# Optimization experiments

Measured on AMD Instinct MI355X. Metric: run time of the kernel, lower is better.

The kernel has to match this reference:

```python
import jax, jax.numpy as jnp
import numpy as np

# Scatter2Operator config (matches init_kwargs)
NUM_HEADS = 16   # dims[2] / glob_size
GLOB_SIZE = 64
HEAD_SIZE = 64   # dims[2] / num_heads


def setup_inputs() -> dict:
    key = jax.random.key(0)
    ks = jax.random.split(key, 6)
    B, N, G, D0, D2 = 8, 4096, 64, 1024, 1024
    scale = 0.02
    return {
        "x0": jax.random.normal(ks[0], (B, G, D0), jnp.float32),
        "x2": jax.random.normal(ks[1], (B, N, D2), jnp.float32),
        "Wk": jax.random.normal(ks[2], (NUM_HEADS * GLOB_SIZE, D2), jnp.float32) * scale,
        "Wp": jax.random.normal(ks[3], (NUM_HEADS * HEAD_SIZE, D0), jnp.float32) * scale,
        "Wo": jax.random.normal(ks[4], (D2, NUM_HEADS * HEAD_SIZE), jnp.float32) * scale,
        "bo": jnp.zeros((D2,), jnp.float32),
    }


def reference(x0, x2, Wk, Wp, Wo, bo):
    # x2: [B, N, D2] -> kernel scores; x0: [B, G, D0] -> premise values.
    B, N, _ = x2.shape
    H, G, Dh = NUM_HEADS, GLOB_SIZE, HEAD_SIZE
    # kernel = softmax over glob slots (dropout is identity in eval mode)
    k = jnp.einsum('bnd,kd->bnk', x2, Wk).reshape(B, N, H, G)
    k = jax.nn.softmax(k, axis=-1)                      # [B, N, H, G]
    # premise projection: [B, G, H, Dh]
    p = jnp.einsum('bgd,kd->bgk', x0, Wp).reshape(B, G, H, Dh)
    # attention-like gather over the G global slots, per head
    pred = jnp.einsum('bnhg,bghd->bnhd', k, p)          # [B, N, H, Dh]
    pred = pred.reshape(B, N, H * Dh)
    # writer linear (with bias)
    return jnp.einsum('bnk,dk->bnd', pred, Wo) + bo
```

## Files before the change

### kernel.cpp

```cpp
#include <hip/hip_runtime.h>


using bf16x8 = __attribute__((ext_vector_type(8))) __bf16;
using f32x4  = __attribute__((ext_vector_type(4))) float;

__device__ __forceinline__ unsigned short f2b(float f) {
  unsigned u = __float_as_uint(f);
  u += 0x7fffu + ((u >> 16) & 1u);
  return (unsigned short)(u >> 16);
}

__global__ void cvt_all(const float* __restrict__ x2, unsigned short* __restrict__ x2b, int n0,
                        const float* __restrict__ x0, unsigned short* __restrict__ x0b, int n1,
                        const float* __restrict__ Wk, unsigned short* __restrict__ Wkb, int n2,
                        const float* __restrict__ Wp, unsigned short* __restrict__ Wpb, int n3,
                        const float* __restrict__ Wo, unsigned short* __restrict__ Wob, int n4)
{
  const int ntot = n0 + n1 + n2 + n3 + n4;
  int i = blockIdx.x * blockDim.x + threadIdx.x;
  const int stride = gridDim.x * blockDim.x;
  for (; i < ntot; i += stride) {
    const float* src; unsigned short* dst; int j = i;
    if (j < n0) { src = x2; dst = x2b; }
    else if ((j -= n0) < n1) { src = x0; dst = x0b; }
    else if ((j -= n1) < n2) { src = Wk; dst = Wkb; }
    else if ((j -= n2) < n3) { src = Wp; dst = Wpb; }
    else { j -= n3; src = Wo; dst = Wob; }
    float4 v = reinterpret_cast<const float4*>(src)[j];
    ushort4 o;
    o.x = f2b(v.x); o.y = f2b(v.y); o.z = f2b(v.z); o.w = f2b(v.w);
    reinterpret_cast<ushort4*>(dst)[j] = o;
  }
}

#define GLOAD_LDS(gsrc, ldst) __builtin_amdgcn_global_load_lds(                 \
    (const __attribute__((address_space(1))) unsigned int*)(gsrc),              \
    (__attribute__((address_space(3))) unsigned int*)(ldst), 16, 0, 0)

__device__ __forceinline__ void glds16(const unsigned short* g, unsigned ldsoff) {
  asm volatile("s_mov_b32 m0, %0\n\t"
               "global_load_lds_dwordx4 %1, off"
               :: "s"(ldsoff), "v"(g) : "memory");
}

#define BM 128
#define BN 128
#define BK 32

template<int EPI>
__launch_bounds__(256)
__global__ void gemm_bt(const unsigned short* __restrict__ A,
                        const unsigned short* __restrict__ B,
                        void* __restrict__ Cv,
                        const float* __restrict__ bias,
                        int M, int N, int K, int lda, int ldb, int ldc,
                        int batch2,
                        long sA1, long sA2, long sB1, long sB2, long sC1, long sC2)
{
  __shared__ __align__(16) unsigned short As[BM * BK];
  __shared__ __align__(16) unsigned short Bs[BN * BK];

  const int z  = blockIdx.z;
  const int z1 = z / batch2, z2 = z - z1 * batch2;
  const unsigned short* Ab = A + z1 * sA1 + z2 * sA2;
  const unsigned short* Bb = B + z1 * sB1 + z2 * sB2;
  const long cbase = z1 * sC1 + z2 * sC2;

  const int tid  = threadIdx.x;
  const int lane = tid & 63;
  const int wid  = tid >> 6;
  const int wr   = (wid >> 1) * 64;
  const int wc   = (wid & 1) * 64;
  const int brow = blockIdx.x * BM;
  const int bcol = blockIdx.y * BN;
  const int lr   = lane & 15;
  const int ko   = (lane >> 4) * 8;

  f32x4 acc[4][4] = {};

  const int t1  = tid + 256;
  const int r0  = tid >> 2, kc0 = (tid & 3) * 8;
  const int r1  = t1 >> 2,  kc1 = (t1 & 3) * 8;
  int ar0 = brow + r0; if (ar0 >= M) ar0 = M - 1;
  int ar1 = brow + r1; if (ar1 >= M) ar1 = M - 1;
  int br0 = bcol + r0; if (br0 >= N) br0 = N - 1;
  int br1 = bcol + r1; if (br1 >= N) br1 = N - 1;
  const unsigned short* a0p = Ab + (long)ar0 * lda + kc0;
  const unsigned short* a1p = Ab + (long)ar1 * lda + kc1;
  const unsigned short* b0p = Bb + (long)br0 * ldb + kc0;
  const unsigned short* b1p = Bb + (long)br1 * ldb + kc1;

  for (int kt = 0; kt < K; kt += BK) {
    __syncthreads();
    GLOAD_LDS(a0p + kt, &As[tid * 8]);
    GLOAD_LDS(a1p + kt, &As[t1 * 8]);
    GLOAD_LDS(b0p + kt, &Bs[tid * 8]);
    GLOAD_LDS(b1p + kt, &Bs[t1 * 8]);
    __syncthreads();

    bf16x8 af[4], bfr[4];
#pragma unroll
    for (int m = 0; m < 4; ++m)
      af[m] = *reinterpret_cast<const bf16x8*>(&As[(wr + m * 16 + lr) * BK + ko]);
#pragma unroll
    for (int n = 0; n < 4; ++n)
      bfr[n] = *reinterpret_cast<const bf16x8*>(&Bs[(wc + n * 16 + lr) * BK + ko]);
#pragma unroll
    for (int m = 0; m < 4; ++m)
#pragma unroll
      for (int n = 0; n < 4; ++n)
        acc[m][n] = __builtin_amdgcn_mfma_f32_16x16x32_bf16(af[m], bfr[n], acc[m][n], 0, 0, 0);
  }

  const int rowb = brow + wr + (lane >> 4) * 4;
  const int colb = bcol + wc + lr;

  if (EPI == 1) {
    float* C = (float*)Cv + cbase;
#pragma unroll
    for (int n = 0; n < 4; ++n) {
      int col = colb + n * 16;
      if (col >= N) continue;
      float bv = bias ? bias[col] : 0.0f;
#pragma unroll
      for (int m = 0; m < 4; ++m)
#pragma unroll
        for (int r = 0; r < 4; ++r) {
          int row = rowb + m * 16 + r;
          if (row < M) C[(long)row * ldc + col] = acc[m][n][r] + bv;
        }
    }
  } else {
    unsigned short* C = (unsigned short*)Cv + cbase;
#pragma unroll
    for (int n = 0; n < 4; ++n) {
      int col = colb + n * 16;
      if (col >= N) continue;
#pragma unroll
      for (int m = 0; m < 4; ++m)
#pragma unroll
        for (int r = 0; r < 4; ++r) {
          int row = rowb + m * 16 + r;
          if (row < M) C[(long)row * ldc + col] = f2b(acc[m][n][r]);
        }
    }
  }
}


#define BARRIER() __builtin_amdgcn_s_barrier()
#define VMC4()   asm volatile("s_waitcnt vmcnt(4)" ::: "memory")
#define VMC0()   asm volatile("s_waitcnt vmcnt(0)" ::: "memory")


__launch_bounds__(512)
__global__ void gemm256_g1p(const unsigned short* __restrict__ A0,
                            const unsigned short* __restrict__ B0,
                            unsigned short* __restrict__ C0,
                            const unsigned short* __restrict__ A1,
                            const unsigned short* __restrict__ B1,
                            unsigned short* __restrict__ C1,
                            int K)
{
  extern __shared__ __align__(16) char smem[];

  const int tid  = threadIdx.x;
  const int lane = tid & 63, wid = tid >> 6;
  const int wm = wid >> 2, wn = wid & 3;
  const int lr = lane & 15, hi = lane >> 4;
  const int swz  = (lane & 7) << 4;
  const int prow = lane >> 3;
  const int pxor = ((lane & 7) ^ prow) * 8;

  const int bid = blockIdx.x;
  int bx, by, epi;
  const unsigned short* Ab; const unsigned short* Bb; unsigned short* Cb;
  if (bid < 512) {
    const int lin = (bid & 7) * 64 + (bid >> 3);
    bx = lin >> 2; by = lin & 3;
    epi = 2; Ab = A0; Bb = B0; Cb = C0;
  } else {
    const int r = bid - 512;
    bx = r >> 2; by = r & 3;
    epi = 0; Ab = A1; Bb = B1; Cb = C1;
  }
  const int brow = bx * 256, bcol = by * 256;

  unsigned short* ldsA[2] = { (unsigned short*)(smem),
                              (unsigned short*)(smem + 65536) };
  unsigned short* ldsB[2] = { (unsigned short*)(smem + 32768),
                              (unsigned short*)(smem + 98304) };
  const unsigned ldsbase =
      __builtin_amdgcn_readfirstlane((unsigned)(unsigned long long)smem);

  const long ldaL = 1024, ldbL = 1024, ldcL = 1024;

  auto stageA = [&](int buf, int h, int kt) {
    const unsigned short* s = Ab + (long)(brow + h * 128 + wid * 8 + prow) * ldaL + kt + pxor;
    unsigned d = ldsbase + (unsigned)(buf * 65536 + h * 16384 + wid * 1024);
    glds16(s, __builtin_amdgcn_readfirstlane(d));
    glds16(s + 64 * ldaL, __builtin_amdgcn_readfirstlane(d + 8192u));
  };
  auto stageB = [&](int buf, int h, int kt) {
    const unsigned short* s = Bb + (long)(bcol + h * 128 + wid * 8 + prow) * ldbL + kt + pxor;
    unsigned d = ldsbase + (unsigned)(32768 + buf * 65536 + h * 16384 + wid * 1024);
    glds16(s, __builtin_amdgcn_readfirstlane(d));
    glds16(s + 64 * ldbL, __builtin_amdgcn_readfirstlane(d + 8192u));
  };

  bf16x8 afr[4][2], bfr[4][2];
  auto ldA_ = [&](int buf, int mh) {
    const unsigned short* base = ldsA[buf];
#pragma unroll
    for (int mi = 0; mi < 4; ++mi) {
      const int row = wm * 128 + mh * 64 + mi * 16 + lr;
#pragma unroll
      for (int ks = 0; ks < 2; ++ks) {
        const int cb = (ks * 64 + hi * 16) ^ swz;
        afr[mi][ks] = *(const bf16x8*)(base + row * 64 + (cb >> 1));
      }
    }
  };
  auto ldB_ = [&](int buf, int nh) {
    const unsigned short* base = ldsB[buf];
#pragma unroll
    for (int ni = 0; ni < 2; ++ni) {
      const int row = wn * 64 + nh * 32 + ni * 16 + lr;
#pragma unroll
      for (int ks = 0; ks < 2; ++ks) {
        const int cb = (ks * 64 + hi * 16) ^ swz;
        bfr[nh * 2 + ni][ks] = *(const bf16x8*)(base + row * 64 + (cb >> 1));
      }
    }
  };

  f32x4 acc[8][4] = {};
  auto mmaQ = [&](int mh, int nh) {
    __builtin_amdgcn_s_setprio(1);
#pragma unroll
    for (int ks = 0; ks < 2; ++ks)
#pragma unroll
      for (int mi = 0; mi < 4; ++mi)
#pragma unroll
        for (int ni = 0; ni < 2; ++ni)
          acc[mh * 4 + mi][nh * 2 + ni] = __builtin_amdgcn_mfma_f32_16x16x32_bf16(
              afr[mi][ks], bfr[nh * 2 + ni][ks], acc[mh * 4 + mi][nh * 2 + ni], 0, 0, 0);
    __builtin_amdgcn_s_setprio(0);
  };

  stageB(0, 0, 0); stageB(0, 1, 0); stageA(0, 0, 0); stageA(0, 1, 0);
  stageB(1, 0, 64); stageB(1, 1, 64);
  VMC4(); BARRIER();

  const int NI = K >> 7;
#pragma unroll 1
  for (int i = 0; i < NI; ++i) {
    const int kt1 = i * 128 + 64;
    int kt2 = i * 128 + 128; if (kt2 >= K) kt2 -= K;
    int kt3 = i * 128 + 192; if (kt3 >= K) kt3 -= K;

    ldA_(0, 0); ldB_(0, 0); ldB_(0, 1); stageA(1, 0, kt1);
    BARRIER(); mmaQ(0, 0); BARRIER();
    stageA(1, 1, kt1);
    BARRIER(); mmaQ(0, 1); BARRIER();
    ldA_(0, 1); stageB(0, 0, kt2);
    BARRIER(); mmaQ(1, 0); BARRIER();
    stageB(0, 1, kt2); VMC4();
    BARRIER(); mmaQ(1, 1); BARRIER();
    ldA_(1, 0); ldB_(1, 0); ldB_(1, 1); stageA(0, 0, kt2);
    BARRIER(); mmaQ(0, 0); BARRIER();
    stageA(0, 1, kt2);
    BARRIER(); mmaQ(0, 1); BARRIER();
    ldA_(1, 1); stageB(1, 0, kt3);
    BARRIER(); mmaQ(1, 0); BARRIER();
    stageB(1, 1, kt3); VMC4();
    BARRIER(); mmaQ(1, 1); BARRIER();
  }
  VMC0();

  const int rowb = brow + wm * 128 + hi * 4;
  const int colb = bcol + wn * 64 + lr;

  if (epi == 2) {
#pragma unroll
    for (int m = 0; m < 8; ++m) {
#pragma unroll
      for (int r = 0; r < 4; ++r) {
        float v0 = acc[m][0][r], v1 = acc[m][1][r], v2 = acc[m][2][r], v3 = acc[m][3][r];
        float mx = fmaxf(fmaxf(v0, v1), fmaxf(v2, v3));
        mx = fmaxf(mx, __shfl_xor(mx, 1));
        mx = fmaxf(mx, __shfl_xor(mx, 2));
        mx = fmaxf(mx, __shfl_xor(mx, 4));
        mx = fmaxf(mx, __shfl_xor(mx, 8));
        float e0 = __expf(v0 - mx), e1 = __expf(v1 - mx);
        float e2 = __expf(v2 - mx), e3 = __expf(v3 - mx);
        float s = e0 + e1 + e2 + e3;
        s += __shfl_xor(s, 1);
        s += __shfl_xor(s, 2);
        s += __shfl_xor(s, 4);
        s += __shfl_xor(s, 8);
        float inv = 1.0f / s;
        unsigned short* cp = Cb + (long)(rowb + m * 16 + r) * ldcL + colb;
        cp[0]  = f2b(e0 * inv);
        cp[16] = f2b(e1 * inv);
        cp[32] = f2b(e2 * inv);
        cp[48] = f2b(e3 * inv);
      }
    }
  } else {
#pragma unroll
    for (int n = 0; n < 4; ++n) {
      const int col = colb + n * 16;
#pragma unroll
      for (int m = 0; m < 8; ++m)
#pragma unroll
        for (int r = 0; r < 4; ++r)
          Cb[(long)(rowb + m * 16 + r) * ldcL + col] = f2b(acc[m][n][r]);
    }
  }
}

__launch_bounds__(512)
__global__ void gemm256_out(const unsigned short* __restrict__ A,
                            const unsigned short* __restrict__ B,
                            float* __restrict__ C,
                            const float* __restrict__ bias,
                            int K, long sA, long sB, long sC)
{
  extern __shared__ __align__(16) char smem[];

  const int tid  = threadIdx.x;
  const int lane = tid & 63, wid = tid >> 6;
  const int wm = wid >> 2, wn = wid & 3;
  const int lr = lane & 15, hi = lane >> 4;
  const int swz  = (lane & 7) << 4;
  const int prow = lane >> 3;
  const int pxor = ((lane & 7) ^ prow) * 8;

  const int bid = blockIdx.x;
  const int z = bid & 7, idx = bid >> 3;
  const int bx = idx & 15, by = idx >> 4;
  const int brow = bx * 256, bcol = by * 256;
  const unsigned short* __restrict__ Ab = A + (long)z * sA;
  const unsigned short* __restrict__ Bb = B + (long)z * sB;
  const long cbase = (long)z * sC;

  unsigned short* ldsA[2] = { (unsigned short*)(smem),
                              (unsigned short*)(smem + 65536) };
  unsigned short* ldsB[2] = { (unsigned short*)(smem + 32768),
                              (unsigned short*)(smem + 98304) };
  const unsigned ldsbase =
      __builtin_amdgcn_readfirstlane((unsigned)(unsigned long long)smem);

  const long ldaL = 1024, ldbL = 1024, ldcL = 1024;

  auto stageA = [&](int buf, int h, int kt) {
    const unsigned short* s = Ab + (long)(brow + h * 128 + wid * 8 + prow) * ldaL + kt + pxor;
    unsigned d = ldsbase + (unsigned)(buf * 65536 + h * 16384 + wid * 1024);
    glds16(s, __builtin_amdgcn_readfirstlane(d));
    glds16(s + 64 * ldaL, __builtin_amdgcn_readfirstlane(d + 8192u));
  };
  auto stageB = [&](int buf, int h, int kt) {
    const unsigned short* s = Bb + (long)(bcol + h * 128 + wid * 8 + prow) * ldbL + kt + pxor;
    unsigned d = ldsbase + (unsigned)(32768 + buf * 65536 + h * 16384 + wid * 1024);
    glds16(s, __builtin_amdgcn_readfirstlane(d));
    glds16(s + 64 * ldbL, __builtin_amdgcn_readfirstlane(d + 8192u));
  };

  bf16x8 afr[4][2], bfr[4][2];
  auto ldA_ = [&](int buf, int mh) {
    const unsigned short* base = ldsA[buf];
#pragma unroll
    for (int mi = 0; mi < 4; ++mi) {
      const int row = wm * 128 + mh * 64 + mi * 16 + lr;
#pragma unroll
      for (int ks = 0; ks < 2; ++ks) {
        const int cb = (ks * 64 + hi * 16) ^ swz;
        afr[mi][ks] = *(const bf16x8*)(base + row * 64 + (cb >> 1));
      }
    }
  };
  auto ldB_ = [&](int buf, int nh) {
    const unsigned short* base = ldsB[buf];
#pragma unroll
    for (int ni = 0; ni < 2; ++ni) {
      const int row = wn * 64 + nh * 32 + ni * 16 + lr;
#pragma unroll
      for (int ks = 0; ks < 2; ++ks) {
        const int cb = (ks * 64 + hi * 16) ^ swz;
        bfr[nh * 2 + ni][ks] = *(const bf16x8*)(base + row * 64 + (cb >> 1));
      }
    }
  };

  f32x4 acc[8][4] = {};
  auto mmaQ = [&](int mh, int nh) {
    __builtin_amdgcn_s_setprio(1);
#pragma unroll
    for (int ks = 0; ks < 2; ++ks)
#pragma unroll
      for (int mi = 0; mi < 4; ++mi)
#pragma unroll
        for (int ni = 0; ni < 2; ++ni)
          acc[mh * 4 + mi][nh * 2 + ni] = __builtin_amdgcn_mfma_f32_16x16x32_bf16(
              afr[mi][ks], bfr[nh * 2 + ni][ks], acc[mh * 4 + mi][nh * 2 + ni], 0, 0, 0);
    __builtin_amdgcn_s_setprio(0);
  };

  stageB(0, 0, 0); stageB(0, 1, 0); stageA(0, 0, 0); stageA(0, 1, 0);
  stageB(1, 0, 64); stageB(1, 1, 64);
  VMC4(); BARRIER();

  const int NI = K >> 7;
#pragma unroll 1
  for (int i = 0; i < NI; ++i) {
    const int kt1 = i * 128 + 64;
    int kt2 = i * 128 + 128; if (kt2 >= K) kt2 -= K;
    int kt3 = i * 128 + 192; if (kt3 >= K) kt3 -= K;

    ldA_(0, 0); ldB_(0, 0); ldB_(0, 1); stageA(1, 0, kt1);
    BARRIER(); mmaQ(0, 0); BARRIER();
    stageA(1, 1, kt1);
    BARRIER(); mmaQ(0, 1); BARRIER();
    ldA_(0, 1); stageB(0, 0, kt2);
    BARRIER(); mmaQ(1, 0); BARRIER();
    stageB(0, 1, kt2); VMC4();
    BARRIER(); mmaQ(1, 1); BARRIER();
    ldA_(1, 0); ldB_(1, 0); ldB_(1, 1); stageA(0, 0, kt2);
    BARRIER(); mmaQ(0, 0); BARRIER();
    stageA(0, 1, kt2);
    BARRIER(); mmaQ(0, 1); BARRIER();
    ldA_(1, 1); stageB(1, 0, kt3);
    BARRIER(); mmaQ(1, 0); BARRIER();
    stageB(1, 1, kt3); VMC4();
    BARRIER(); mmaQ(1, 1); BARRIER();
  }
  VMC0();

  const int rowb = brow + wm * 128 + hi * 4;
  const int colb = bcol + wn * 64 + lr;
  float* Co = C + cbase;
#pragma unroll
  for (int n = 0; n < 4; ++n) {
    const int col = colb + n * 16;
    const float bv = bias[col];
#pragma unroll
    for (int m = 0; m < 8; ++m)
#pragma unroll
      for (int r = 0; r < 4; ++r)
        Co[(long)(rowb + m * 16 + r) * ldcL + col] = acc[m][n][r] + bv;
  }
}

extern "C" void kernel_launch(void* const* d_in, const int* in_sizes, int n_in,
                              void* d_out, int out_size, void* d_ws, size_t ws_size,
                              hipStream_t stream) {
  (void)in_sizes; (void)n_in; (void)out_size; (void)ws_size;
  const float* x0 = (const float*)d_in[0];
  const float* x2 = (const float*)d_in[1];
  const float* Wk = (const float*)d_in[2];
  const float* Wp = (const float*)d_in[3];
  const float* Wo = (const float*)d_in[4];
  const float* bo = (const float*)d_in[5];
  float* out = (float*)d_out;

  const long Bz = 8, Nn = 4096, Gg = 64, Dd = 1024;
  const long MN = Bz * Nn;

  char* ws = (char*)d_ws;
  size_t off = 0;
  auto alloc = [&](size_t bytes) {
    size_t cur = off;
    off = (cur + bytes + 255) & ~(size_t)255;
    return (unsigned short*)(ws + cur);
  };
  unsigned short* x2b = alloc(MN * Dd * 2);
  unsigned short* kb  = alloc(MN * Dd * 2);
  unsigned short* Wkb = alloc(Dd * Dd * 2);
  unsigned short* Wpb = alloc(Dd * Dd * 2);
  unsigned short* Wob = alloc(Dd * Dd * 2);
  unsigned short* x0b = alloc(Bz * Gg * Dd * 2);
  unsigned short* Pb  = alloc(Bz * Gg * Dd * 2);
  unsigned short* Qtb = alloc(Bz * Dd * Dd * 2);

  hipFuncSetAttribute(reinterpret_cast<const void*>(gemm256_g1p),
                      hipFuncAttributeMaxDynamicSharedMemorySize, 131072);
  hipFuncSetAttribute(reinterpret_cast<const void*>(gemm256_out),
                      hipFuncAttributeMaxDynamicSharedMemorySize, 131072);

  cvt_all<<<dim3(4096), dim3(256), 0, stream>>>(
      x2, x2b, (int)(MN * Dd / 4),
      x0, x0b, (int)(Bz * Gg * Dd / 4),
      Wk, Wkb, (int)(Dd * Dd / 4),
      Wp, Wpb, (int)(Dd * Dd / 4),
      Wo, Wob, (int)(Dd * Dd / 4));

  gemm256_g1p<<<dim3(520, 1, 1), dim3(512), 131072, stream>>>(
      x2b, Wkb, kb, x0b, Wpb, Pb, 1024);

  gemm_bt<0><<<dim3(8, 1, 128), dim3(256), 0, stream>>>(
      Wob, Pb, Qtb, nullptr, 1024, 64, 64, 1024, 1024, 1024,
      16, 0, 64, 65536, 64, 1048576, 64);

  gemm256_out<<<dim3(512, 1, 1), dim3(512), 131072, stream>>>(
      kb, Qtb, out, bo, 1024,
      (long)4096 * 1024, (long)1024 * 1024, (long)4096 * 1024);
}
```

Baseline: 239.0 us.

## Double-buffer register fragments and restructure GEMM main loop prefetch schedule

Splits the A and B register fragments into separate ping-pong sets so the next quarter's LDS reads are issued before the current MFMA block rather than immediately after it. Global-to-LDS staging is regrouped in pairs per phase with adjusted vmcnt waits, and the prologue preloads the first fragments. Launch bounds now request two waves per SIMD. The aim is to hide LDS read latency behind MFMAs, at the cost of more VGPRs under a tighter register cap, which may cause spills. The buffer reuse pattern across barriers must stay race-free.

```diff
diff --git a/kernel.cpp b/kernel.cpp
--- a/kernel.cpp
+++ b/kernel.cpp
@@ -147,13 +147,11 @@
   }
 }
 
-
 #define BARRIER() __builtin_amdgcn_s_barrier()
 #define VMC4()   asm volatile("s_waitcnt vmcnt(4)" ::: "memory")
 #define VMC0()   asm volatile("s_waitcnt vmcnt(0)" ::: "memory")
 
-
-__launch_bounds__(512)
+__launch_bounds__(512, 2)
 __global__ void gemm256_g1p(const unsigned short* __restrict__ A0,
                             const unsigned short* __restrict__ B0,
                             unsigned short* __restrict__ C0,
@@ -208,8 +206,10 @@
     glds16(s + 64 * ldbL, __builtin_amdgcn_readfirstlane(d + 8192u));
   };
 
-  bf16x8 afr[4][2], bfr[4][2];
-  auto ldA_ = [&](int buf, int mh) {
+  bf16x8 afr0[4][2], afr1[4][2];
+  bf16x8 bloA[2][2], bloB[2][2], bhi[2][2];
+
+  auto ldA = [&](int buf, int mh, bf16x8 (&dst)[4][2]) {
     const unsigned short* base = ldsA[buf];
 #pragma unroll
     for (int mi = 0; mi < 4; ++mi) {
@@ -217,11 +217,11 @@
 #pragma unroll
       for (int ks = 0; ks < 2; ++ks) {
         const int cb = (ks * 64 + hi * 16) ^ swz;
-        afr[mi][ks] = *(const bf16x8*)(base + row * 64 + (cb >> 1));
+        dst[mi][ks] = *(const bf16x8*)(base + row * 64 + (cb >> 1));
       }
     }
   };
-  auto ldB_ = [&](int buf, int nh) {
+  auto ldB = [&](int buf, int nh, bf16x8 (&dst)[2][2]) {
     const unsigned short* base = ldsB[buf];
 #pragma unroll
     for (int ni = 0; ni < 2; ++ni) {
@@ -229,13 +229,13 @@
 #pragma unroll
       for (int ks = 0; ks < 2; ++ks) {
         const int cb = (ks * 64 + hi * 16) ^ swz;
-        bfr[nh * 2 + ni][ks] = *(const bf16x8*)(base + row * 64 + (cb >> 1));
+        dst[ni][ks] = *(const bf16x8*)(base + row * 64 + (cb >> 1));
       }
     }
   };
 
   f32x4 acc[8][4] = {};
-  auto mmaQ = [&](int mh, int nh) {
+  auto mma = [&](bf16x8 (&a)[4][2], bf16x8 (&b)[2][2], int mh, int nh) {
     __builtin_amdgcn_s_setprio(1);
 #pragma unroll
     for (int ks = 0; ks < 2; ++ks)
@@ -244,13 +244,14 @@
 #pragma unroll
         for (int ni = 0; ni < 2; ++ni)
           acc[mh * 4 + mi][nh * 2 + ni] = __builtin_amdgcn_mfma_f32_16x16x32_bf16(
-              afr[mi][ks], bfr[nh * 2 + ni][ks], acc[mh * 4 + mi][nh * 2 + ni], 0, 0, 0);
+              a[mi][ks], b[ni][ks], acc[mh * 4 + mi][nh * 2 + ni], 0, 0, 0);
     __builtin_amdgcn_s_setprio(0);
   };
 
-  stageB(0, 0, 0); stageB(0, 1, 0); stageA(0, 0, 0); stageA(0, 1, 0);
+  stageA(0, 0, 0); stageA(0, 1, 0); stageB(0, 0, 0); stageB(0, 1, 0);
   stageB(1, 0, 64); stageB(1, 1, 64);
-  VMC4(); BARRIER();
+  VMC0(); BARRIER();
+  ldA(0, 0, afr0); ldB(0, 0, bloA);
 
   const int NI = K >> 7;
 #pragma unroll 1
@@ -259,22 +260,26 @@
     int kt2 = i * 128 + 128; if (kt2 >= K) kt2 -= K;
     int kt3 = i * 128 + 192; if (kt3 >= K) kt3 -= K;
 
-    ldA_(0, 0); ldB_(0, 0); ldB_(0, 1); stageA(1, 0, kt1);
-    BARRIER(); mmaQ(0, 0); BARRIER();
-    stageA(1, 1, kt1);
-    BARRIER(); mmaQ(0, 1); BARRIER();
-    ldA_(0, 1); stageB(0, 0, kt2);
-    BARRIER(); mmaQ(1, 0); BARRIER();
-    stageB(0, 1, kt2); VMC4();
-    BARRIER(); mmaQ(1, 1); BARRIER();
-    ldA_(1, 0); ldB_(1, 0); ldB_(1, 1); stageA(0, 0, kt2);
-    BARRIER(); mmaQ(0, 0); BARRIER();
-    stageA(0, 1, kt2);
-    BARRIER(); mmaQ(0, 1); BARRIER();
-    ldA_(1, 1); stageB(1, 0, kt3);
-    BARRIER(); mmaQ(1, 0); BARRIER();
-    stageB(1, 1, kt3); VMC4();
-    BARRIER(); mmaQ(1, 1); BARRIER();
+    ldB(0, 1, bhi);
+    stageA(1, 0, kt1); stageA(1, 1, kt1); VMC4();
+    BARRIER(); mma(afr0, bloA, 0, 0); BARRIER();
+    ldA(0, 1, afr1);
+    BARRIER(); mma(afr0, bhi, 0, 1); BARRIER();
+    ldB(1, 0, bloB);
+    stageB(0, 0, kt2); stageB(0, 1, kt2); VMC4();
+    BARRIER(); mma(afr1, bloA, 1, 0); BARRIER();
+    ldA(1, 0, afr0);
+    BARRIER(); mma(afr1, bhi, 1, 1); BARRIER();
+    ldB(1, 1, bhi);
+    stageA(0, 0, kt2); stageA(0, 1, kt2); VMC4();
+    BARRIER(); mma(afr0, bloB, 0, 0); BARRIER();
+    ldA(1, 1, afr1);
+    BARRIER(); mma(afr0, bhi, 0, 1); BARRIER();
+    ldB(0, 0, bloA);
+    stageB(1, 0, kt3); stageB(1, 1, kt3); VMC4();
+    BARRIER(); mma(afr1, bloB, 1, 0); BARRIER();
+    ldA(0, 0, afr0);
+    BARRIER(); mma(afr1, bhi, 1, 1); BARRIER();
   }
   VMC0();
 
```

Result: slower. 254.3 us (+6.4%).

## Fuse premise projection into Qt kernel, drop extra blocks from score GEMM

Applied to the files above, without the earlier changes.

The premise projection P = x0·Wp^T, which was computed by 8 extra blocks appended to the score GEMM, moves into a new qtp kernel. qtp computes each per-(batch, head) 64x64 P tile in LDS and immediately multiplies it with a 256-row slice of Wo to produce Qt. This removes the P round-trip through global memory and the generic 128x128 batched GEMM with its padded/clamped tiles, and lets the score GEMM run a uniform 512-block grid. In exchange, each of the 4 bx blocks per (b, h) recomputes the same P tile, which is redundant work.

```diff
diff --git a/kernel.cpp b/kernel.cpp
--- a/kernel.cpp
+++ b/kernel.cpp
@@ -43,124 +43,144 @@
                :: "s"(ldsoff), "v"(g) : "memory");
 }
 
-#define BM 128
-#define BN 128
-#define BK 32
-
-template<int EPI>
+#define BARRIER() __builtin_amdgcn_s_barrier()
+#define VMC4()   asm volatile("s_waitcnt vmcnt(4)" ::: "memory")
+#define VMC0()   asm volatile("s_waitcnt vmcnt(0)" ::: "memory")
+
 __launch_bounds__(256)
-__global__ void gemm_bt(const unsigned short* __restrict__ A,
-                        const unsigned short* __restrict__ B,
-                        void* __restrict__ Cv,
-                        const float* __restrict__ bias,
-                        int M, int N, int K, int lda, int ldb, int ldc,
-                        int batch2,
-                        long sA1, long sA2, long sB1, long sB2, long sC1, long sC2)
+__global__ void qtp(const unsigned short* __restrict__ x0b,
+                    const unsigned short* __restrict__ Wpb,
+                    const unsigned short* __restrict__ Wob,
+                    unsigned short* __restrict__ Qtb)
 {
-  __shared__ __align__(16) unsigned short As[BM * BK];
-  __shared__ __align__(16) unsigned short Bs[BN * BK];
-
+  __shared__ __align__(16) unsigned short Pl[64 * 72];
+  __shared__ __align__(16) unsigned short work[16384];
+
+  const int bx = blockIdx.x;
   const int z  = blockIdx.z;
-  const int z1 = z / batch2, z2 = z - z1 * batch2;
-  const unsigned short* Ab = A + z1 * sA1 + z2 * sA2;
-  const unsigned short* Bb = B + z1 * sB1 + z2 * sB2;
-  const long cbase = z1 * sC1 + z2 * sC2;
+  const int b  = z >> 4, h = z & 15;
 
   const int tid  = threadIdx.x;
   const int lane = tid & 63;
   const int wid  = tid >> 6;
-  const int wr   = (wid >> 1) * 64;
-  const int wc   = (wid & 1) * 64;
-  const int brow = blockIdx.x * BM;
-  const int bcol = blockIdx.y * BN;
   const int lr   = lane & 15;
-  const int ko   = (lane >> 4) * 8;
-
-  f32x4 acc[4][4] = {};
-
-  const int t1  = tid + 256;
-  const int r0  = tid >> 2, kc0 = (tid & 3) * 8;
-  const int r1  = t1 >> 2,  kc1 = (t1 & 3) * 8;
-  int ar0 = brow + r0; if (ar0 >= M) ar0 = M - 1;
-  int ar1 = brow + r1; if (ar1 >= M) ar1 = M - 1;
-  int br0 = bcol + r0; if (br0 >= N) br0 = N - 1;
-  int br1 = bcol + r1; if (br1 >= N) br1 = N - 1;
-  const unsigned short* a0p = Ab + (long)ar0 * lda + kc0;
-  const unsigned short* a1p = Ab + (long)ar1 * lda + kc1;
-  const unsigned short* b0p = Bb + (long)br0 * ldb + kc0;
-  const unsigned short* b1p = Bb + (long)br1 * ldb + kc1;
-
-  for (int kt = 0; kt < K; kt += BK) {
+  const int hi   = lane >> 4;
+
+  const int wr1 = (wid >> 1) * 32, wc1 = (wid & 1) * 32;
+  f32x4 acc1[2][2] = {};
+
+  int srow[2], skc[2];
+#pragma unroll
+  for (int j = 0; j < 2; ++j) {
+    int i = j * 256 + tid;
+    srow[j] = i >> 3;
+    skc[j]  = ((i & 7) ^ (srow[j] & 7)) * 8;
+  }
+  const unsigned short* aSrc = x0b + (long)b * 65536;
+  const unsigned short* bSrc = Wpb + (long)h * 64 * 1024;
+
+  for (int kt = 0; kt < 1024; kt += 64) {
     __syncthreads();
-    GLOAD_LDS(a0p + kt, &As[tid * 8]);
-    GLOAD_LDS(a1p + kt, &As[t1 * 8]);
-    GLOAD_LDS(b0p + kt, &Bs[tid * 8]);
-    GLOAD_LDS(b1p + kt, &Bs[t1 * 8]);
+#pragma unroll
+    for (int j = 0; j < 2; ++j) {
+      int i = j * 256 + tid;
+      GLOAD_LDS(aSrc + (long)srow[j] * 1024 + kt + skc[j], &work[i * 8]);
+      GLOAD_LDS(bSrc + (long)srow[j] * 1024 + kt + skc[j], &work[4096 + i * 8]);
+    }
     __syncthreads();
 
-    bf16x8 af[4], bfr[4];
+    bf16x8 af[2][2], bf[2][2];
+#pragma unroll
+    for (int m = 0; m < 2; ++m) {
+      const int rowA = wr1 + m * 16 + lr;
+      const int rowB = wc1 + m * 16 + lr;
+#pragma unroll
+      for (int ks = 0; ks < 2; ++ks) {
+        const int slotA = ((ks * 4 + hi) ^ (rowA & 7)) * 8;
+        const int slotB = ((ks * 4 + hi) ^ (rowB & 7)) * 8;
+        af[m][ks] = *(const bf16x8*)&work[rowA * 64 + slotA];
+        bf[m][ks] = *(const bf16x8*)&work[4096 + rowB * 64 + slotB];
+      }
+    }
+#pragma unroll
+    for (int ks = 0; ks < 2; ++ks)
+#pragma unroll
+      for (int m = 0; m < 2; ++m)
+#pragma unroll
+        for (int n = 0; n < 2; ++n)
+          acc1[m][n] = __builtin_amdgcn_mfma_f32_16x16x32_bf16(
+              af[m][ks], bf[n][ks], acc1[m][n], 0, 0, 0);
+  }
+
+#pragma unroll
+  for (int m = 0; m < 2; ++m)
+#pragma unroll
+    for (int r = 0; r < 4; ++r) {
+      const int row = wr1 + m * 16 + hi * 4 + r;
+#pragma unroll
+      for (int n = 0; n < 2; ++n)
+        Pl[row * 72 + wc1 + n * 16 + lr] = f2b(acc1[m][n][r]);
+    }
+  __syncthreads();
+
+  const unsigned short* wSrc = Wob + (long)bx * 256 * 1024 + h * 64;
+#pragma unroll
+  for (int j = 0; j < 8; ++j) {
+    int i = j * 256 + tid;
+    int row = i >> 3;
+    int kc  = ((i & 7) ^ (row & 7)) * 8;
+    GLOAD_LDS(wSrc + (long)row * 1024 + kc, &work[i * 8]);
+  }
+  __syncthreads();
+
+  const int wr2 = wid * 64;
+  f32x4 acc2[4][4] = {};
+  bf16x8 af2[4][2], bf2[4][2];
+#pragma unroll
+  for (int m = 0; m < 4; ++m) {
+    const int rowA = wr2 + m * 16 + lr;
+#pragma unroll
+    for (int ks = 0; ks < 2; ++ks) {
+      const int slotA = ((ks * 4 + hi) ^ (rowA & 7)) * 8;
+      af2[m][ks] = *(const bf16x8*)&work[rowA * 64 + slotA];
+    }
+  }
+#pragma unroll
+  for (int n = 0; n < 4; ++n) {
+    const int rowB = n * 16 + lr;
+#pragma unroll
+    for (int ks = 0; ks < 2; ++ks)
+      bf2[n][ks] = *(const bf16x8*)&Pl[rowB * 72 + ks * 32 + hi * 8];
+  }
+#pragma unroll
+  for (int ks = 0; ks < 2; ++ks)
 #pragma unroll
     for (int m = 0; m < 4; ++m)
-      af[m] = *reinterpret_cast<const bf16x8*>(&As[(wr + m * 16 + lr) * BK + ko]);
-#pragma unroll
-    for (int n = 0; n < 4; ++n)
-      bfr[n] = *reinterpret_cast<const bf16x8*>(&Bs[(wc + n * 16 + lr) * BK + ko]);
+#pragma unroll
+      for (int n = 0; n < 4; ++n)
+        acc2[m][n] = __builtin_amdgcn_mfma_f32_16x16x32_bf16(
+            af2[m][ks], bf2[n][ks], acc2[m][n], 0, 0, 0);
+
+  unsigned short* Cq = Qtb + (long)b * 1048576 + h * 64;
+#pragma unroll
+  for (int n = 0; n < 4; ++n) {
+    const int col = n * 16 + lr;
 #pragma unroll
     for (int m = 0; m < 4; ++m)
 #pragma unroll
-      for (int n = 0; n < 4; ++n)
-        acc[m][n] = __builtin_amdgcn_mfma_f32_16x16x32_bf16(af[m], bfr[n], acc[m][n], 0, 0, 0);
-  }
-
-  const int rowb = brow + wr + (lane >> 4) * 4;
-  const int colb = bcol + wc + lr;
-
-  if (EPI == 1) {
-    float* C = (float*)Cv + cbase;
-#pragma unroll
-    for (int n = 0; n < 4; ++n) {
-      int col = colb + n * 16;
-      if (col >= N) continue;
-      float bv = bias ? bias[col] : 0.0f;
-#pragma unroll
-      for (int m = 0; m < 4; ++m)
-#pragma unroll
-        for (int r = 0; r < 4; ++r) {
-          int row = rowb + m * 16 + r;
-          if (row < M) C[(long)row * ldc + col] = acc[m][n][r] + bv;
-        }
-    }
-  } else {
-    unsigned short* C = (unsigned short*)Cv + cbase;
-#pragma unroll
-    for (int n = 0; n < 4; ++n) {
-      int col = colb + n * 16;
-      if (col >= N) continue;
-#pragma unroll
-      for (int m = 0; m < 4; ++m)
-#pragma unroll
-        for (int r = 0; r < 4; ++r) {
-          int row = rowb + m * 16 + r;
-          if (row < M) C[(long)row * ldc + col] = f2b(acc[m][n][r]);
-        }
-    }
-  }
-}
-
-
-#define BARRIER() __builtin_amdgcn_s_barrier()
-#define VMC4()   asm volatile("s_waitcnt vmcnt(4)" ::: "memory")
-#define VMC0()   asm volatile("s_waitcnt vmcnt(0)" ::: "memory")
+      for (int r = 0; r < 4; ++r) {
+        const int row = bx * 256 + wr2 + m * 16 + hi * 4 + r;
+        Cq[(long)row * 1024 + col] = f2b(acc2[m][n][r]);
+      }
+  }
+}
 
 
 __launch_bounds__(512)
-__global__ void gemm256_g1p(const unsigned short* __restrict__ A0,
-                            const unsigned short* __restrict__ B0,
-                            unsigned short* __restrict__ C0,
-                            const unsigned short* __restrict__ A1,
-                            const unsigned short* __restrict__ B1,
-                            unsigned short* __restrict__ C1,
-                            int K)
+__global__ void gemm256_g1(const unsigned short* __restrict__ A,
+                           const unsigned short* __restrict__ B,
+                           unsigned short* __restrict__ C,
+                           int K)
 {
   extern __shared__ __align__(16) char smem[];
 
@@ -173,17 +193,8 @@
   const int pxor = ((lane & 7) ^ prow) * 8;
 
   const int bid = blockIdx.x;
-  int bx, by, epi;
-  const unsigned short* Ab; const unsigned short* Bb; unsigned short* Cb;
-  if (bid < 512) {
-    const int lin = (bid & 7) * 64 + (bid >> 3);
-    bx = lin >> 2; by = lin & 3;
-    epi = 2; Ab = A0; Bb = B0; Cb = C0;
-  } else {
-    const int r = bid - 512;
-    bx = r >> 2; by = r & 3;
-    epi = 0; Ab = A1; Bb = B1; Cb = C1;
-  }
+  const int lin = (bid & 7) * 64 + (bid >> 3);
+  const int bx = lin >> 2, by = lin & 3;
   const int brow = bx * 256, bcol = by * 256;
 
   unsigned short* ldsA[2] = { (unsigned short*)(smem),
@@ -196,13 +207,13 @@
   const long ldaL = 1024, ldbL = 1024, ldcL = 1024;
 
   auto stageA = [&](int buf, int h, int kt) {
-    const unsigned short* s = Ab + (long)(brow + h * 128 + wid * 8 + prow) * ldaL + kt + pxor;
+    const unsigned short* s = A + (long)(brow + h * 128 + wid * 8 + prow) * ldaL + kt + pxor;
     unsigned d = ldsbase + (unsigned)(buf * 65536 + h * 16384 + wid * 1024);
     glds16(s, __builtin_amdgcn_readfirstlane(d));
     glds16(s + 64 * ldaL, __builtin_amdgcn_readfirstlane(d + 8192u));
   };
   auto stageB = [&](int buf, int h, int kt) {
-    const unsigned short* s = Bb + (long)(bcol + h * 128 + wid * 8 + prow) * ldbL + kt + pxor;
+    const unsigned short* s = B + (long)(bcol + h * 128 + wid * 8 + prow) * ldbL + kt + pxor;
     unsigned d = ldsbase + (unsigned)(32768 + buf * 65536 + h * 16384 + wid * 1024);
     glds16(s, __builtin_amdgcn_readfirstlane(d));
     glds16(s + 64 * ldbL, __builtin_amdgcn_readfirstlane(d + 8192u));
@@ -280,42 +291,29 @@
 
   const int rowb = brow + wm * 128 + hi * 4;
   const int colb = bcol + wn * 64 + lr;
-
-  if (epi == 2) {
-#pragma unroll
-    for (int m = 0; m < 8; ++m) {
-#pragma unroll
-      for (int r = 0; r < 4; ++r) {
-        float v0 = acc[m][0][r], v1 = acc[m][1][r], v2 = acc[m][2][r], v3 = acc[m][3][r];
-        float mx = fmaxf(fmaxf(v0, v1), fmaxf(v2, v3));
-        mx = fmaxf(mx, __shfl_xor(mx, 1));
-        mx = fmaxf(mx, __shfl_xor(mx, 2));
-        mx = fmaxf(mx, __shfl_xor(mx, 4));
-        mx = fmaxf(mx, __shfl_xor(mx, 8));
-        float e0 = __expf(v0 - mx), e1 = __expf(v1 - mx);
-        float e2 = __expf(v2 - mx), e3 = __expf(v3 - mx);
-        float s = e0 + e1 + e2 + e3;
-        s += __shfl_xor(s, 1);
-        s += __shfl_xor(s, 2);
-        s += __shfl_xor(s, 4);
-        s += __shfl_xor(s, 8);
-        float inv = 1.0f / s;
-        unsigned short* cp = Cb + (long)(rowb + m * 16 + r) * ldcL + colb;
-        cp[0]  = f2b(e0 * inv);
-        cp[16] = f2b(e1 * inv);
-        cp[32] = f2b(e2 * inv);
-        cp[48] = f2b(e3 * inv);
-      }
-    }
-  } else {
-#pragma unroll
-    for (int n = 0; n < 4; ++n) {
-      const int col = colb + n * 16;
-#pragma unroll
-      for (int m = 0; m < 8; ++m)
-#pragma unroll
-        for (int r = 0; r < 4; ++r)
-          Cb[(long)(rowb + m * 16 + r) * ldcL + col] = f2b(acc[m][n][r]);
+#pragma unroll
+  for (int m = 0; m < 8; ++m) {
+#pragma unroll
+    for (int r = 0; r < 4; ++r) {
+      float v0 = acc[m][0][r], v1 = acc[m][1][r], v2 = acc[m][2][r], v3 = acc[m][3][r];
+      float mx = fmaxf(fmaxf(v0, v1), fmaxf(v2, v3));
+      mx = fmaxf(mx, __shfl_xor(mx, 1));
+      mx = fmaxf(mx, __shfl_xor(mx, 2));
+      mx = fmaxf(mx, __shfl_xor(mx, 4));
+      mx = fmaxf(mx, __shfl_xor(mx, 8));
+      float e0 = __expf(v0 - mx), e1 = __expf(v1 - mx);
+      float e2 = __expf(v2 - mx), e3 = __expf(v3 - mx);
+      float s = e0 + e1 + e2 + e3;
+      s += __shfl_xor(s, 1);
+      s += __shfl_xor(s, 2);
+      s += __shfl_xor(s, 4);
+      s += __shfl_xor(s, 8);
+      float inv = 1.0f / s;
+      unsigned short* cp = C + (long)(rowb + m * 16 + r) * ldcL + colb;
+      cp[0]  = f2b(e0 * inv);
+      cp[16] = f2b(e1 * inv);
+      cp[32] = f2b(e2 * inv);
+      cp[48] = f2b(e3 * inv);
     }
   }
 }
@@ -480,10 +478,9 @@
   unsigned short* Wpb = alloc(Dd * Dd * 2);
   unsigned short* Wob = alloc(Dd * Dd * 2);
   unsigned short* x0b = alloc(Bz * Gg * Dd * 2);
-  unsigned short* Pb  = alloc(Bz * Gg * Dd * 2);
   unsigned short* Qtb = alloc(Bz * Dd * Dd * 2);
 
-  hipFuncSetAttribute(reinterpret_cast<const void*>(gemm256_g1p),
+  hipFuncSetAttribute(reinterpret_cast<const void*>(gemm256_g1),
                       hipFuncAttributeMaxDynamicSharedMemorySize, 131072);
   hipFuncSetAttribute(reinterpret_cast<const void*>(gemm256_out),
                       hipFuncAttributeMaxDynamicSharedMemorySize, 131072);
@@ -495,12 +492,10 @@
       Wp, Wpb, (int)(Dd * Dd / 4),
       Wo, Wob, (int)(Dd * Dd / 4));
 
-  gemm256_g1p<<<dim3(520, 1, 1), dim3(512), 131072, stream>>>(
-      x2b, Wkb, kb, x0b, Wpb, Pb, 1024);
-
-  gemm_bt<0><<<dim3(8, 1, 128), dim3(256), 0, stream>>>(
-      Wob, Pb, Qtb, nullptr, 1024, 64, 64, 1024, 1024, 1024,
-      16, 0, 64, 65536, 64, 1048576, 64);
+  gemm256_g1<<<dim3(512, 1, 1), dim3(512), 131072, stream>>>(
+      x2b, Wkb, kb, 1024);
+
+  qtp<<<dim3(4, 1, 128), dim3(256), 0, stream>>>(x0b, Wpb, Wob, Qtb);
 
   gemm256_out<<<dim3(512, 1, 1), dim3(512), 131072, stream>>>(
       kb, Qtb, out, bo, 1024,
```

Measured after the change: 220.8 us. 7.6% less time.
